# Optimization experiments

Measured on AMD Instinct MI355X. Metric: run time of the kernel, lower is better.

## Reference

```python
import jax, jax.numpy as jnp
import numpy as np

NUM_HEADS = 8
NUM_LEVELS = 4
NUM_POINTS = 16
NUM_BEV = 2
EMBED = 256
BS = 64
NQ = NUM_LEVELS * NUM_POINTS  # 64


def _bilinear_sample(img, grid):
    """F.grid_sample(mode='bilinear', padding_mode='zeros', align_corners=False).
    img: (N, C, H, W); grid: (N, Hg, Wg, 2) in [-1, 1] (x, y). Returns (N, C, Hg, Wg)."""
    N, C, H, W = img.shape
    gx = (grid[..., 0] + 1.0) * (W * 0.5) - 0.5  # (N, Hg, Wg)
    gy = (grid[..., 1] + 1.0) * (H * 0.5) - 0.5
    x0 = jnp.floor(gx)
    y0 = jnp.floor(gy)
    flat = img.reshape(N, C, H * W)

    def gather(xi, yi):
        valid = (xi >= 0) & (xi <= W - 1) & (yi >= 0) & (yi <= H - 1)
        xc = jnp.clip(xi, 0, W - 1).astype(jnp.int32)
        yc = jnp.clip(yi, 0, H - 1).astype(jnp.int32)
        idx = (yc * W + xc).reshape(N, 1, -1)
        g = jnp.take_along_axis(flat, idx, axis=2).reshape(N, C, xi.shape[1], xi.shape[2])
        return g * valid[:, None, :, :].astype(img.dtype)

    wx1 = (gx - x0)[:, None]  # (N,1,Hg,Wg)
    wy1 = (gy - y0)[:, None]
    v00 = gather(x0, y0)
    v01 = gather(x0 + 1.0, y0)
    v10 = gather(x0, y0 + 1.0)
    v11 = gather(x0 + 1.0, y0 + 1.0)
    top = v00 * (1.0 - wx1) + v01 * wx1
    bot = v10 * (1.0 - wx1) + v11 * wx1
    return top * (1.0 - wy1) + bot * wy1


def _forward(query, key_hist, value_hist, reference_points, W_off, b_off, spatial_shapes):
    bs, nq, d = query.shape
    Hn, L, P, BEV = NUM_HEADS, NUM_LEVELS, NUM_POINTS, NUM_BEV
    dh = d // Hn
    Pb = P * BEV
    ss = np.asarray(spatial_shapes)  # (L, 2) static (h, w)

    queries = jnp.concatenate([query, query], axis=1)           # (bs, 2*nq, d)
    keies = jnp.concatenate([query, key_hist], axis=1)
    values = jnp.concatenate([query, value_hist], axis=1)
    qb = queries.shape[1]

    # sampling offsets projection (the only used learned linear in the original forward)
    off = (queries @ W_off + b_off).reshape(bs, qb, Hn, Pb, L, 2)

    # NOTE: original re-assigns q/k/v from the RAW concatenated tensors (to_Q/to_K/to_V discarded)
    qh = queries.reshape(bs, qb, Hn, dh)
    kh = keies.reshape(bs, qb, Hn, dh)
    vh = values.reshape(bs, qb, Hn, dh)

    attn = jax.nn.softmax(jnp.einsum('bqhd,bkhd->bqhk', qh, kh), axis=-1)
    attn = attn.reshape(bs, qb, Hn, L, Pb)

    rp = jnp.concatenate([reference_points, reference_points], axis=1)  # (bs, qb, L, 2)
    norm = jnp.stack([jnp.asarray(ss[:, 1], jnp.float32),
                      jnp.asarray(ss[:, 0], jnp.float32)], axis=-1)      # (L, 2) = (w, h)
    loc = rp[:, :, None, None, :, :] + off / norm                        # (bs,qb,H,Pb,L,2)
    # FAITHFUL: original uses .view here (pure reshape, not a transpose)
    loc = loc.reshape(bs, qb, Hn, L, Pb, 2)
    grids = 2.0 * loc - 1.0

    sampled = []
    start = 0
    for l in range(L):
        h_, w_ = int(ss[l, 0]), int(ss[l, 1])
        vl = vh[:, start:start + h_ * w_]                                # (bs, hw, H, dh)
        start += h_ * w_
        img = vl.transpose(0, 2, 3, 1).reshape(bs * Hn, dh, h_, w_)      # (bs*H, dh, h, w)
        grid_l = grids[:, :, :, l].transpose(0, 2, 1, 3, 4).reshape(bs * Hn, qb, Pb, 2)
        sampled.append(_bilinear_sample(img, grid_l))                    # (bs*H, dh, qb, Pb)

    samp = jnp.stack(sampled, axis=-2).reshape(bs * Hn, dh, qb, L * Pb)
    aw = attn.transpose(0, 2, 1, 3, 4).reshape(bs * Hn, 1, qb, L * Pb)
    out = (samp * aw).sum(-1)                                            # (bs*H, dh, qb)
    # FAITHFUL: original reshapes q_bev dim as (nq, BEV) and means over BEV
    out = out.reshape(bs, Hn * dh, nq, BEV).mean(-1).transpose(0, 2, 1)  # (bs, nq, d)
    return out + query  # dropout is identity at eval


def setup_inputs() -> dict:
    key = jax.random.key(0)
    ks = jax.random.split(key, 6)
    query = jax.random.normal(ks[0], (BS, NQ, EMBED), jnp.float32)
    key_hist = jax.random.normal(ks[1], (BS, NQ, EMBED), jnp.float32)
    value_hist = jax.random.normal(ks[2], (BS, NQ, EMBED), jnp.float32)
    reference_points = jax.random.uniform(ks[3], (BS, NQ, NUM_LEVELS, 2), jnp.float32)
    spatial_shapes = jnp.array([[4, 8]] * NUM_LEVELS, dtype=jnp.int32)  # sum(h*w)=128=L*P*BEV
    off_dim = NUM_HEADS * NUM_BEV * NUM_POINTS * NUM_LEVELS * 2
    W_off = jax.random.normal(ks[4], (EMBED, off_dim), jnp.float32) * 0.02
    b_off = jnp.zeros((off_dim,), jnp.float32)
    return {"query": query, "key_hist": key_hist, "value_hist": value_hist,
            "reference_points": reference_points, "spatial_shapes": spatial_shapes,
            "W_off": W_off, "b_off": b_off}


def reference(query, key_hist, value_hist, reference_points, spatial_shapes, W_off, b_off):
    return _forward(query, key_hist, value_hist, reference_points, W_off, b_off, spatial_shapes)
```

## Files before the change

kernel.cpp:

```cpp
#include <hip/hip_runtime.h>


typedef short  s16x8 __attribute__((ext_vector_type(8)));
typedef short  s16x4 __attribute__((ext_vector_type(4)));
typedef float  f32x4 __attribute__((ext_vector_type(4)));

__device__ __forceinline__ unsigned short f2bf(float f) {
    union { float f; unsigned u; } v; v.f = f;
    unsigned r = v.u + 0x7FFFu + ((v.u >> 16) & 1u);
    return (unsigned short)(r >> 16);
}

__global__ __launch_bounds__(256) void conv_bf16(const float* __restrict__ in,
                                                 short* __restrict__ out) {
    const int i4 = (blockIdx.x * 256 + threadIdx.x) * 4;
    const float4 v = *(const float4*)(in + i4);
    s16x4 o;
    o.x = (short)f2bf(v.x); o.y = (short)f2bf(v.y);
    o.z = (short)f2bf(v.z); o.w = (short)f2bf(v.w);
    *(s16x4*)(out + i4) = o;
}

__global__ __launch_bounds__(256) void transp_bf16(const float* __restrict__ W,
                                                   short* __restrict__ Wt) {
    __shared__ float s[32][33];
    const int n0 = blockIdx.x * 32, k0 = blockIdx.y * 32;
    const int c = threadIdx.x & 31, r0 = threadIdx.x >> 5;
    #pragma unroll
    for (int p = 0; p < 4; ++p) {
        const int r = r0 + p * 8;
        s[r][c] = W[(size_t)(k0 + r) * 2048 + n0 + c];
    }
    __syncthreads();
    #pragma unroll
    for (int p = 0; p < 4; ++p) {
        const int r = r0 + p * 8;
        Wt[(size_t)(n0 + r) * 256 + k0 + c] = (short)f2bf(s[c][r]);
    }
}

__global__ __launch_bounds__(256) void offs_gemm_mfma(
    const short* __restrict__ Ab, const short* __restrict__ Wt,
    const float* __restrict__ bias, short* __restrict__ OFFb)
{
    __shared__ __align__(16) short Asl[128][40];
    __shared__ __align__(16) short Bsl[128][40];
    const int n0 = blockIdx.x * 128, m0 = blockIdx.y * 128;
    const int t = threadIdx.x, lane = t & 63, wave = t >> 6;
    const int wm0 = (wave >> 1) * 64, wn0 = (wave & 1) * 64;
    const int r = lane & 15, q = lane >> 4;

    f32x4 acc[4][4] = {};

    for (int kc = 0; kc < 256; kc += 32) {
        #pragma unroll
        for (int ss = 0; ss < 2; ++ss) {
            const int seg = t + ss * 256;
            const int row = seg >> 2, off8 = (seg & 3) * 8;
            *(s16x8*)&Asl[row][off8] =
                *(const s16x8*)(Ab + (size_t)(m0 + row) * 256 + kc + off8);
            *(s16x8*)&Bsl[row][off8] =
                *(const s16x8*)(Wt + (size_t)(n0 + row) * 256 + kc + off8);
        }
        __syncthreads();
        s16x8 af[4], bf[4];
        #pragma unroll
        for (int i = 0; i < 4; ++i) {
            af[i] = *(const s16x8*)&Asl[wm0 + i * 16 + r][q * 8];
            bf[i] = *(const s16x8*)&Bsl[wn0 + i * 16 + r][q * 8];
        }
        #pragma unroll
        for (int i = 0; i < 4; ++i)
            #pragma unroll
            for (int j = 0; j < 4; ++j)
                acc[i][j] = __builtin_amdgcn_mfma_f32_16x16x32_bf16(
                    af[i], bf[j], acc[i][j], 0, 0, 0);
        __syncthreads();
    }

    #pragma unroll
    for (int j = 0; j < 4; ++j) {
        const int col = n0 + wn0 + j * 16 + r;
        const float bb = bias[col];
        #pragma unroll
        for (int i = 0; i < 4; ++i) {
            const int rowg = m0 + wm0 + i * 16 + q * 4;
            #pragma unroll
            for (int rg = 0; rg < 4; ++rg)
                OFFb[(size_t)(rowg + rg) * 2048 + col] =
                    (short)f2bf(acc[i][j][rg] + bb);
        }
    }
}

__global__ __launch_bounds__(256, 2) void fused_tsa(
    const float* __restrict__ query, const float* __restrict__ key_hist,
    const float* __restrict__ value_hist, const float* __restrict__ refp,
    const unsigned short* __restrict__ OFFb, float* __restrict__ out)
{
    const int h  = blockIdx.x;
    const int b  = blockIdx.y;
    const int s  = blockIdx.z;
    const int q0 = s * 32;
    const int t  = threadIdx.x;

    __shared__ float pool[32 * 128 + 32 * 32];
    __shared__ float vs[128][36];
    __shared__ float att[32][128];
    __shared__ float rps[32][8];
    __shared__ float red[32][8];
    __shared__ float rowmax[32];
    __shared__ float invsum[32];

    float (*ks_t)[128] = (float (*)[128])pool;
    float (*qs_t)[32]  = (float (*)[32])(pool + 4096);
    float (*Am)[132]   = (float (*)[132])pool;

    {
        const int q = t & 31, v4 = t >> 5;
        const float4 v = *(const float4*)(query +
            (size_t)(b * 64 + q0 + q) * 256 + h * 32 + v4 * 4);
        qs_t[v4 * 4 + 0][q] = v.x; qs_t[v4 * 4 + 1][q] = v.y;
        qs_t[v4 * 4 + 2][q] = v.z; qs_t[v4 * 4 + 3][q] = v.w;
    }
    {
        const int kq = t & 31, v4 = t >> 5;
        #pragma unroll
        for (int p = 0; p < 4; ++p) {
            const int krow = p * 32 + kq;
            const size_t roff = (krow < 64)
                ? (size_t)(b * 64 + krow) * 256
                : (size_t)(b * 64 + krow - 64) * 256;
            const float* srck = (krow < 64) ? query : key_hist;
            const float* srcv = (krow < 64) ? query : value_hist;
            const float4 kv = *(const float4*)(srck + roff + h * 32 + v4 * 4);
            ks_t[v4 * 4 + 0][krow] = kv.x; ks_t[v4 * 4 + 1][krow] = kv.y;
            ks_t[v4 * 4 + 2][krow] = kv.z; ks_t[v4 * 4 + 3][krow] = kv.w;
            *(float4*)(&vs[krow][v4 * 4]) =
                *(const float4*)(srcv + roff + h * 32 + v4 * 4);
        }
    }
    {
        const int q = t >> 3, j = t & 7;
        rps[q][j] = refp[(size_t)(b * 64 + q0 + q) * 8 + j];
    }
    __syncthreads();

    {
        const int qt = (t >> 5) * 4;
        const int kt = (t & 31) * 4;
        float accl[4][4] = {};
        #pragma unroll
        for (int dd = 0; dd < 32; ++dd) {
            const float4 qv = *(const float4*)(&qs_t[dd][qt]);
            const float4 kv = *(const float4*)(&ks_t[dd][kt]);
            const float qa[4] = {qv.x, qv.y, qv.z, qv.w};
            const float ka[4] = {kv.x, kv.y, kv.z, kv.w};
            #pragma unroll
            for (int i = 0; i < 4; ++i)
                #pragma unroll
                for (int j = 0; j < 4; ++j)
                    accl[i][j] += qa[i] * ka[j];
        }
        #pragma unroll
        for (int i = 0; i < 4; ++i)
            #pragma unroll
            for (int j = 0; j < 4; ++j)
                att[qt + i][kt + j] = accl[i][j];
    }
    __syncthreads();

    for (int idx = t; idx < 32 * 132; idx += 256) pool[idx] = 0.f;

    {
        const int q = t >> 3, part = t & 7;
        const int k0 = part * 16;
        float m = -1e30f;
        #pragma unroll
        for (int k = 0; k < 16; ++k) m = fmaxf(m, att[q][k0 + k]);
        red[q][part] = m;
        __syncthreads();
        if (part == 0) {
            float M = red[q][0];
            #pragma unroll
            for (int p = 1; p < 8; ++p) M = fmaxf(M, red[q][p]);
            rowmax[q] = M;
        }
        __syncthreads();
        const float M = rowmax[q];
        float ssum = 0.f;
        #pragma unroll
        for (int k = 0; k < 16; ++k) {
            const float e = __expf(att[q][k0 + k] - M);
            att[q][k0 + k] = e;
            ssum += e;
        }
        red[q][part] = ssum;
        __syncthreads();
        if (part == 0) {
            float S = red[q][0];
            #pragma unroll
            for (int p = 1; p < 8; ++p) S += red[q][p];
            invsum[q] = 1.0f / S;
        }
        __syncthreads();
    }

    {
        const int q = t >> 3, fg = t & 7;
        const unsigned int* offrow = (const unsigned int*)(OFFb +
            (size_t)(b * 64 + q0 + q) * 2048 + h * 256);
        const float isum = invsum[q];
        float* row = Am[q];
        for (int i = 0; i < 16; ++i) {
            const int f = fg + 8 * i;
            const unsigned int u = offrow[f];
            const float oxv = __uint_as_float(u << 16);
            const float oyv = __uint_as_float(u & 0xFFFF0000u);
            const float a = att[q][f] * isum;
            const int l = f & 3;
            const float locx = rps[q][l * 2 + 0] + oxv * 0.125f;
            const float locy = rps[q][l * 2 + 1] + oyv * 0.25f;
            const float gx = 8.f * locx - 0.5f;
            const float gy = 4.f * locy - 0.5f;
            const float x0f = floorf(gx), y0f = floorf(gy);
            const float wx = gx - x0f, wy = gy - y0f;
            const int x0 = (int)x0f, y0 = (int)y0f;
            const int base = (f >> 5) * 32;
            const bool xv0 = (x0 >= 0) && (x0 < 8);
            const bool xv1 = (x0 >= -1) && (x0 < 7);
            const bool yv0 = (y0 >= 0) && (y0 < 4);
            const bool yv1 = (y0 >= -1) && (y0 < 3);
            if (xv0 && yv0) atomicAdd(&row[base + y0 * 8 + x0],           a * (1.f - wx) * (1.f - wy));
            if (xv1 && yv0) atomicAdd(&row[base + y0 * 8 + x0 + 1],       a * wx * (1.f - wy));
            if (xv0 && yv1) atomicAdd(&row[base + (y0 + 1) * 8 + x0],     a * (1.f - wx) * wy);
            if (xv1 && yv1) atomicAdd(&row[base + (y0 + 1) * 8 + x0 + 1], a * wx * wy);
        }
    }
    __syncthreads();

    {
        const int d4 = (t & 7) * 4;
        const int q  = t >> 3;
        float acc[4] = {0.f, 0.f, 0.f, 0.f};
        #pragma unroll 4
        for (int p = 0; p < 128; ++p) {
            const float a = Am[q][p];
            const float4 v = *(const float4*)(&vs[p][d4]);
            acc[0] += a * v.x; acc[1] += a * v.y;
            acc[2] += a * v.z; acc[3] += a * v.w;
        }
        float avg[4];
        #pragma unroll
        for (int j = 0; j < 4; ++j)
            avg[j] = 0.5f * (acc[j] + __shfl_xor(acc[j], 8, 64));
        const int qg  = q0 + q;
        const int pj  = qg >> 1;
        const int row = (qg & 1) ? (pj + 32) : pj;
        const float4 qv = *(const float4*)(query +
            (size_t)(b * 64 + row) * 256 + h * 32 + d4);
        float4 o;
        o.x = qv.x + avg[0]; o.y = qv.y + avg[1];
        o.z = qv.z + avg[2]; o.w = qv.w + avg[3];
        *(float4*)(out + (size_t)(b * 64 + row) * 256 + h * 32 + d4) = o;
    }
}

extern "C" void kernel_launch(void* const* d_in, const int* in_sizes, int n_in,
                              void* d_out, int out_size, void* d_ws, size_t ws_size,
                              hipStream_t stream) {
    (void)in_sizes; (void)n_in; (void)out_size; (void)ws_size;
    const float* query      = (const float*)d_in[0];
    const float* key_hist   = (const float*)d_in[1];
    const float* value_hist = (const float*)d_in[2];
    const float* refp       = (const float*)d_in[3];
    const float* W_off      = (const float*)d_in[5];
    const float* b_off      = (const float*)d_in[6];

    char* ws = (char*)d_ws;
    short* Ab   = (short*)(ws);
    short* Wt   = (short*)(ws + (2u << 20));
    short* OFFb = (short*)(ws + (3u << 20));
    float* out  = (float*)d_out;

    conv_bf16<<<1024, 256, 0, stream>>>(query, Ab);
    transp_bf16<<<dim3(64, 8), 256, 0, stream>>>(W_off, Wt);
    offs_gemm_mfma<<<dim3(16, 32), 256, 0, stream>>>(Ab, Wt, b_off, OFFb);
    fused_tsa<<<dim3(8, 64, 2), 256, 0, stream>>>(query, key_hist, value_hist,
                                                  refp, (const unsigned short*)OFFb,
                                                  out);
}
```

Measured before the change: 178.4 us.

## Restructure pipeline: MFMA attention and value GEMM, fused W conversion, staged stores

The two prep kernels are merged into one. It converts query and key_hist to bf16 and builds a transposed bf16 copy of the values. The offset GEMM now reads fp32 W directly, converting and transposing it in-tile, and writes its output through LDS so global stores are coalesced. The main kernel handles all 64 queries per (batch, head) block and computes QK^T and the sample-weighted value product with MFMA bf16 instructions, doing the softmax in registers with shuffles. This removes the scalar FP32 dot-product loops and several syncs, at the cost of reduced precision in scores and values and a fresh W conversion in every GEMM block.

New measurement: 187.3 us. 5.0% more time.

```diff
diff --git a/kernel.cpp b/kernel.cpp
--- a/kernel.cpp
+++ b/kernel.cpp
@@ -11,40 +11,51 @@
     return (unsigned short)(r >> 16);
 }
 
-__global__ __launch_bounds__(256) void conv_bf16(const float* __restrict__ in,
-                                                 short* __restrict__ out) {
-    const int i4 = (blockIdx.x * 256 + threadIdx.x) * 4;
-    const float4 v = *(const float4*)(in + i4);
-    s16x4 o;
-    o.x = (short)f2bf(v.x); o.y = (short)f2bf(v.y);
-    o.z = (short)f2bf(v.z); o.w = (short)f2bf(v.w);
-    *(s16x4*)(out + i4) = o;
-}
-
-__global__ __launch_bounds__(256) void transp_bf16(const float* __restrict__ W,
-                                                   short* __restrict__ Wt) {
-    __shared__ float s[32][33];
-    const int n0 = blockIdx.x * 32, k0 = blockIdx.y * 32;
-    const int c = threadIdx.x & 31, r0 = threadIdx.x >> 5;
-    #pragma unroll
-    for (int p = 0; p < 4; ++p) {
-        const int r = r0 + p * 8;
-        s[r][c] = W[(size_t)(k0 + r) * 2048 + n0 + c];
-    }
-    __syncthreads();
-    #pragma unroll
-    for (int p = 0; p < 4; ++p) {
-        const int r = r0 + p * 8;
-        Wt[(size_t)(n0 + r) * 256 + k0 + c] = (short)f2bf(s[c][r]);
+__global__ __launch_bounds__(256) void prep(
+    const float* __restrict__ query, const float* __restrict__ key_hist,
+    const float* __restrict__ value_hist,
+    short* __restrict__ Ab, short* __restrict__ Khb, short* __restrict__ VTg)
+{
+    const int job = blockIdx.x, t = threadIdx.x;
+    if (job < 2048) {
+        const bool isK = job >= 1024;
+        const float* src = isK ? key_hist : query;
+        short* dst = isK ? Khb : Ab;
+        const int i4 = ((job & 1023) * 256 + t) * 4;
+        const float4 v = *(const float4*)(src + i4);
+        s16x4 o;
+        o.x = (short)f2bf(v.x); o.y = (short)f2bf(v.y);
+        o.z = (short)f2bf(v.z); o.w = (short)f2bf(v.w);
+        *(s16x4*)(dst + i4) = o;
+    } else {
+        const int bh = job - 2048;
+        const int b = bh >> 3, h = bh & 7;
+        #pragma unroll
+        for (int pass = 0; pass < 4; ++pass) {
+            const int idx = t + 256 * pass;
+            const int p = idx >> 3;
+            const int dg = idx & 7;
+            const float* src = (p < 64) ? query : value_hist;
+            const float4 v = *(const float4*)(src +
+                (size_t)(b * 64 + (p & 63)) * 256 + h * 32 + dg * 4);
+            short* o = VTg + ((size_t)bh * 32 + dg * 4) * 128 + p;
+            o[0 * 128] = (short)f2bf(v.x);
+            o[1 * 128] = (short)f2bf(v.y);
+            o[2 * 128] = (short)f2bf(v.z);
+            o[3 * 128] = (short)f2bf(v.w);
+        }
     }
 }
 
 __global__ __launch_bounds__(256) void offs_gemm_mfma(
-    const short* __restrict__ Ab, const short* __restrict__ Wt,
+    const short* __restrict__ Ab, const float* __restrict__ W,
     const float* __restrict__ bias, short* __restrict__ OFFb)
 {
-    __shared__ __align__(16) short Asl[128][40];
-    __shared__ __align__(16) short Bsl[128][40];
+    __shared__ __align__(16) short smem[128 * 136];
+    short (*Asl)[40] = (short (*)[40])smem;
+    short (*Bsl)[40] = (short (*)[40])(smem + 128 * 40);
+    short (*Cst)[136] = (short (*)[136])smem;
+
     const int n0 = blockIdx.x * 128, m0 = blockIdx.y * 128;
     const int t = threadIdx.x, lane = t & 63, wave = t >> 6;
     const int wm0 = (wave >> 1) * 64, wn0 = (wave & 1) * 64;
@@ -59,8 +70,16 @@
             const int row = seg >> 2, off8 = (seg & 3) * 8;
             *(s16x8*)&Asl[row][off8] =
                 *(const s16x8*)(Ab + (size_t)(m0 + row) * 256 + kc + off8);
-            *(s16x8*)&Bsl[row][off8] =
-                *(const s16x8*)(Wt + (size_t)(n0 + row) * 256 + kc + off8);
+        }
+        #pragma unroll
+        for (int i = 0; i < 4; ++i) {
+            const int slot = t + 256 * i;
+            const int kk = slot >> 5, n4 = (slot & 31) * 4;
+            const float4 w4 = *(const float4*)(W + (size_t)(kc + kk) * 2048 + n0 + n4);
+            Bsl[n4 + 0][kk] = (short)f2bf(w4.x);
+            Bsl[n4 + 1][kk] = (short)f2bf(w4.y);
+            Bsl[n4 + 2][kk] = (short)f2bf(w4.z);
+            Bsl[n4 + 3][kk] = (short)f2bf(w4.w);
         }
         __syncthreads();
         s16x8 af[4], bf[4];
@@ -80,189 +99,171 @@
 
     #pragma unroll
     for (int j = 0; j < 4; ++j) {
-        const int col = n0 + wn0 + j * 16 + r;
-        const float bb = bias[col];
-        #pragma unroll
-        for (int i = 0; i < 4; ++i) {
-            const int rowg = m0 + wm0 + i * 16 + q * 4;
+        const float bb = bias[n0 + wn0 + j * 16 + r];
+        #pragma unroll
+        for (int i = 0; i < 4; ++i)
             #pragma unroll
             for (int rg = 0; rg < 4; ++rg)
-                OFFb[(size_t)(rowg + rg) * 2048 + col] =
+                Cst[wm0 + i * 16 + q * 4 + rg][wn0 + j * 16 + r] =
                     (short)f2bf(acc[i][j][rg] + bb);
-        }
-    }
-}
-
-__global__ __launch_bounds__(256, 2) void fused_tsa(
-    const float* __restrict__ query, const float* __restrict__ key_hist,
-    const float* __restrict__ value_hist, const float* __restrict__ refp,
-    const unsigned short* __restrict__ OFFb, float* __restrict__ out)
+    }
+    __syncthreads();
+    {
+        const int row = t >> 1, half = t & 1;
+        short* gdst = OFFb + (size_t)(m0 + row) * 2048 + n0 + half * 64;
+        const short* lsrc = &Cst[row][half * 64];
+        #pragma unroll
+        for (int u = 0; u < 8; ++u)
+            *(s16x8*)(gdst + u * 8) = *(const s16x8*)(lsrc + u * 8);
+    }
+}
+
+__global__ __launch_bounds__(256) void fused_tsa2(
+    const float* __restrict__ query, const float* __restrict__ refp,
+    const short* __restrict__ Ab, const short* __restrict__ Khb,
+    const short* __restrict__ VTg, const unsigned* __restrict__ OFFu,
+    float* __restrict__ out)
 {
-    const int h  = blockIdx.x;
-    const int b  = blockIdx.y;
-    const int s  = blockIdx.z;
-    const int q0 = s * 32;
-    const int t  = threadIdx.x;
-
-    __shared__ float pool[32 * 128 + 32 * 32];
-    __shared__ float vs[128][36];
-    __shared__ float att[32][128];
-    __shared__ float rps[32][8];
-    __shared__ float red[32][8];
-    __shared__ float rowmax[32];
-    __shared__ float invsum[32];
-
-    float (*ks_t)[128] = (float (*)[128])pool;
-    float (*qs_t)[32]  = (float (*)[32])(pool + 4096);
-    float (*Am)[132]   = (float (*)[132])pool;
-
-    {
-        const int q = t & 31, v4 = t >> 5;
-        const float4 v = *(const float4*)(query +
-            (size_t)(b * 64 + q0 + q) * 256 + h * 32 + v4 * 4);
-        qs_t[v4 * 4 + 0][q] = v.x; qs_t[v4 * 4 + 1][q] = v.y;
-        qs_t[v4 * 4 + 2][q] = v.z; qs_t[v4 * 4 + 3][q] = v.w;
-    }
-    {
-        const int kq = t & 31, v4 = t >> 5;
-        #pragma unroll
-        for (int p = 0; p < 4; ++p) {
-            const int krow = p * 32 + kq;
-            const size_t roff = (krow < 64)
-                ? (size_t)(b * 64 + krow) * 256
-                : (size_t)(b * 64 + krow - 64) * 256;
-            const float* srck = (krow < 64) ? query : key_hist;
-            const float* srcv = (krow < 64) ? query : value_hist;
-            const float4 kv = *(const float4*)(srck + roff + h * 32 + v4 * 4);
-            ks_t[v4 * 4 + 0][krow] = kv.x; ks_t[v4 * 4 + 1][krow] = kv.y;
-            ks_t[v4 * 4 + 2][krow] = kv.z; ks_t[v4 * 4 + 3][krow] = kv.w;
-            *(float4*)(&vs[krow][v4 * 4]) =
-                *(const float4*)(srcv + roff + h * 32 + v4 * 4);
-        }
-    }
-    {
-        const int q = t >> 3, j = t & 7;
-        rps[q][j] = refp[(size_t)(b * 64 + q0 + q) * 8 + j];
-    }
-    __syncthreads();
-
-    {
-        const int qt = (t >> 5) * 4;
-        const int kt = (t & 31) * 4;
-        float accl[4][4] = {};
-        #pragma unroll
-        for (int dd = 0; dd < 32; ++dd) {
-            const float4 qv = *(const float4*)(&qs_t[dd][qt]);
-            const float4 kv = *(const float4*)(&ks_t[dd][kt]);
-            const float qa[4] = {qv.x, qv.y, qv.z, qv.w};
-            const float ka[4] = {kv.x, kv.y, kv.z, kv.w};
-            #pragma unroll
-            for (int i = 0; i < 4; ++i)
-                #pragma unroll
-                for (int j = 0; j < 4; ++j)
-                    accl[i][j] += qa[i] * ka[j];
-        }
-        #pragma unroll
-        for (int i = 0; i < 4; ++i)
-            #pragma unroll
-            for (int j = 0; j < 4; ++j)
-                att[qt + i][kt + j] = accl[i][j];
-    }
-    __syncthreads();
-
-    for (int idx = t; idx < 32 * 132; idx += 256) pool[idx] = 0.f;
-
-    {
-        const int q = t >> 3, part = t & 7;
-        const int k0 = part * 16;
-        float m = -1e30f;
-        #pragma unroll
-        for (int k = 0; k < 16; ++k) m = fmaxf(m, att[q][k0 + k]);
-        red[q][part] = m;
-        __syncthreads();
-        if (part == 0) {
-            float M = red[q][0];
-            #pragma unroll
-            for (int p = 1; p < 8; ++p) M = fmaxf(M, red[q][p]);
-            rowmax[q] = M;
-        }
-        __syncthreads();
-        const float M = rowmax[q];
+    const int h = blockIdx.x, b = blockIdx.y;
+    const int t = threadIdx.x, lane = t & 63, wave = t >> 6;
+    const int quad = lane >> 4, col = lane & 15;
+    const int wq = wave * 16;
+
+    __shared__ __align__(16) float Am[64][132];
+    short* Amb = (short*)&Am[0][0];
+
+    unsigned off_u[8][4];
+    {
+        const unsigned* ob = OFFu + ((size_t)b * 64 + wq + quad * 4) * 1024 + h * 128 + col;
+        #pragma unroll
+        for (int r = 0; r < 4; ++r)
+            #pragma unroll
+            for (int t8 = 0; t8 < 8; ++t8)
+                off_u[t8][r] = ob[r * 1024 + t8 * 16];
+    }
+    float rpx[4], rpy[4];
+    #pragma unroll
+    for (int r = 0; r < 4; ++r) {
+        const float2 rp = *(const float2*)(refp +
+            ((size_t)b * 64 + wq + quad * 4 + r) * 8 + (lane & 3) * 2);
+        rpx[r] = rp.x; rpy[r] = rp.y;
+    }
+
+    {
+        const int zq = t >> 2, zc = (t & 3) * 32;
+        const float4 z = {0.f, 0.f, 0.f, 0.f};
+        #pragma unroll
+        for (int u = 0; u < 8; ++u) *(float4*)&Am[zq][zc + 4 * u] = z;
+    }
+
+    const s16x8 aq = *(const s16x8*)(Ab +
+        ((size_t)b * 64 + wq + col) * 256 + h * 32 + quad * 8);
+    f32x4 acc[8];
+    #pragma unroll
+    for (int t8 = 0; t8 < 8; ++t8) {
+        const int n = t8 * 16 + col;
+        const short* src = (t8 < 4)
+            ? (Ab  + ((size_t)b * 64 + n) * 256)
+            : (Khb + ((size_t)b * 64 + n - 64) * 256);
+        const s16x8 bk = *(const s16x8*)(src + h * 32 + quad * 8);
+        const f32x4 z = {0.f, 0.f, 0.f, 0.f};
+        acc[t8] = __builtin_amdgcn_mfma_f32_16x16x32_bf16(aq, bk, z, 0, 0, 0);
+    }
+
+    float att[8][4];
+    #pragma unroll
+    for (int r = 0; r < 4; ++r) {
+        float m = acc[0][r];
+        #pragma unroll
+        for (int t8 = 1; t8 < 8; ++t8) m = fmaxf(m, acc[t8][r]);
+        #pragma unroll
+        for (int s = 1; s < 16; s <<= 1) m = fmaxf(m, __shfl_xor(m, s, 64));
         float ssum = 0.f;
         #pragma unroll
-        for (int k = 0; k < 16; ++k) {
-            const float e = __expf(att[q][k0 + k] - M);
-            att[q][k0 + k] = e;
-            ssum += e;
-        }
-        red[q][part] = ssum;
-        __syncthreads();
-        if (part == 0) {
-            float S = red[q][0];
-            #pragma unroll
-            for (int p = 1; p < 8; ++p) S += red[q][p];
-            invsum[q] = 1.0f / S;
-        }
-        __syncthreads();
-    }
-
-    {
-        const int q = t >> 3, fg = t & 7;
-        const unsigned int* offrow = (const unsigned int*)(OFFb +
-            (size_t)(b * 64 + q0 + q) * 2048 + h * 256);
-        const float isum = invsum[q];
-        float* row = Am[q];
-        for (int i = 0; i < 16; ++i) {
-            const int f = fg + 8 * i;
-            const unsigned int u = offrow[f];
-            const float oxv = __uint_as_float(u << 16);
-            const float oyv = __uint_as_float(u & 0xFFFF0000u);
-            const float a = att[q][f] * isum;
-            const int l = f & 3;
-            const float locx = rps[q][l * 2 + 0] + oxv * 0.125f;
-            const float locy = rps[q][l * 2 + 1] + oyv * 0.25f;
-            const float gx = 8.f * locx - 0.5f;
-            const float gy = 4.f * locy - 0.5f;
+        for (int t8 = 0; t8 < 8; ++t8) {
+            const float e = __expf(acc[t8][r] - m);
+            att[t8][r] = e; ssum += e;
+        }
+        #pragma unroll
+        for (int s = 1; s < 16; s <<= 1) ssum += __shfl_xor(ssum, s, 64);
+        const float inv = 1.0f / ssum;
+        #pragma unroll
+        for (int t8 = 0; t8 < 8; ++t8) att[t8][r] *= inv;
+    }
+    __syncthreads();
+
+    #pragma unroll
+    for (int t8 = 0; t8 < 8; ++t8) {
+        const int f = col + 16 * t8;
+        const int base = (f >> 5) * 32;
+        #pragma unroll
+        for (int r = 0; r < 4; ++r) {
+            float* rowW = &Am[wq + quad * 4 + r][0];
+            const float a = att[t8][r];
+            const unsigned u = off_u[t8][r];
+            const float ox = __uint_as_float(u << 16);
+            const float oy = __uint_as_float(u & 0xFFFF0000u);
+            const float gx = 8.f * (rpx[r] + ox * 0.125f) - 0.5f;
+            const float gy = 4.f * (rpy[r] + oy * 0.25f) - 0.5f;
             const float x0f = floorf(gx), y0f = floorf(gy);
             const float wx = gx - x0f, wy = gy - y0f;
             const int x0 = (int)x0f, y0 = (int)y0f;
-            const int base = (f >> 5) * 32;
             const bool xv0 = (x0 >= 0) && (x0 < 8);
             const bool xv1 = (x0 >= -1) && (x0 < 7);
             const bool yv0 = (y0 >= 0) && (y0 < 4);
             const bool yv1 = (y0 >= -1) && (y0 < 3);
-            if (xv0 && yv0) atomicAdd(&row[base + y0 * 8 + x0],           a * (1.f - wx) * (1.f - wy));
-            if (xv1 && yv0) atomicAdd(&row[base + y0 * 8 + x0 + 1],       a * wx * (1.f - wy));
-            if (xv0 && yv1) atomicAdd(&row[base + (y0 + 1) * 8 + x0],     a * (1.f - wx) * wy);
-            if (xv1 && yv1) atomicAdd(&row[base + (y0 + 1) * 8 + x0 + 1], a * wx * wy);
-        }
-    }
-    __syncthreads();
-
-    {
-        const int d4 = (t & 7) * 4;
-        const int q  = t >> 3;
-        float acc[4] = {0.f, 0.f, 0.f, 0.f};
-        #pragma unroll 4
-        for (int p = 0; p < 128; ++p) {
-            const float a = Am[q][p];
-            const float4 v = *(const float4*)(&vs[p][d4]);
-            acc[0] += a * v.x; acc[1] += a * v.y;
-            acc[2] += a * v.z; acc[3] += a * v.w;
-        }
-        float avg[4];
-        #pragma unroll
-        for (int j = 0; j < 4; ++j)
-            avg[j] = 0.5f * (acc[j] + __shfl_xor(acc[j], 8, 64));
-        const int qg  = q0 + q;
-        const int pj  = qg >> 1;
-        const int row = (qg & 1) ? (pj + 32) : pj;
-        const float4 qv = *(const float4*)(query +
-            (size_t)(b * 64 + row) * 256 + h * 32 + d4);
-        float4 o;
-        o.x = qv.x + avg[0]; o.y = qv.y + avg[1];
-        o.z = qv.z + avg[2]; o.w = qv.w + avg[3];
-        *(float4*)(out + (size_t)(b * 64 + row) * 256 + h * 32 + d4) = o;
+            if (xv0 && yv0) atomicAdd(&rowW[base + y0 * 8 + x0],           a * (1.f - wx) * (1.f - wy));
+            if (xv1 && yv0) atomicAdd(&rowW[base + y0 * 8 + x0 + 1],       a * wx * (1.f - wy));
+            if (xv0 && yv1) atomicAdd(&rowW[base + (y0 + 1) * 8 + x0],     a * (1.f - wx) * wy);
+            if (xv1 && yv1) atomicAdd(&rowW[base + (y0 + 1) * 8 + x0 + 1], a * wx * wy);
+        }
+    }
+    __syncthreads();
+
+    {
+        const int cq = t >> 2, cc = (t & 3) * 32;
+        float vreg[32];
+        #pragma unroll
+        for (int u = 0; u < 8; ++u) {
+            const float4 v = *(const float4*)&Am[cq][cc + 4 * u];
+            vreg[4 * u + 0] = v.x; vreg[4 * u + 1] = v.y;
+            vreg[4 * u + 2] = v.z; vreg[4 * u + 3] = v.w;
+        }
+        __syncthreads();
+        #pragma unroll
+        for (int u = 0; u < 4; ++u) {
+            s16x8 o;
+            #pragma unroll
+            for (int j = 0; j < 8; ++j) o[j] = (short)f2bf(vreg[u * 8 + j]);
+            *(s16x8*)&Amb[cq * 136 + cc + u * 8] = o;
+        }
+    }
+    __syncthreads();
+
+    f32x4 oacc[2] = {};
+    #pragma unroll
+    for (int ks = 0; ks < 4; ++ks) {
+        const s16x8 af = *(const s16x8*)&Amb[(wq + col) * 136 + ks * 32 + quad * 8];
+        #pragma unroll
+        for (int n2 = 0; n2 < 2; ++n2) {
+            const s16x8 bv = *(const s16x8*)(VTg +
+                ((size_t)(b * 8 + h) * 32 + n2 * 16 + col) * 128 + ks * 32 + quad * 8);
+            oacc[n2] = __builtin_amdgcn_mfma_f32_16x16x32_bf16(af, bv, oacc[n2], 0, 0, 0);
+        }
+    }
+
+    #pragma unroll
+    for (int n2 = 0; n2 < 2; ++n2) {
+        const int d = h * 32 + n2 * 16 + col;
+        #pragma unroll
+        for (int pr = 0; pr < 2; ++pr) {
+            const float avg = 0.5f * (oacc[n2][2 * pr] + oacc[n2][2 * pr + 1]);
+            const int pj = wave * 8 + quad * 2 + pr;
+            const size_t re = ((size_t)b * 64 + pj) * 256 + d;
+            const size_t ro = ((size_t)b * 64 + pj + 32) * 256 + d;
+            out[re] = query[re] + avg;
+            out[ro] = query[ro] + avg;
+        }
     }
 }
 
@@ -279,14 +280,13 @@
 
     char* ws = (char*)d_ws;
     short* Ab   = (short*)(ws);
-    short* Wt   = (short*)(ws + (2u << 20));
-    short* OFFb = (short*)(ws + (3u << 20));
+    short* Khb  = (short*)(ws + (2u << 20));
+    short* VTg  = (short*)(ws + (4u << 20));
+    short* OFFb = (short*)(ws + (8u << 20));
     float* out  = (float*)d_out;
 
-    conv_bf16<<<1024, 256, 0, stream>>>(query, Ab);
-    transp_bf16<<<dim3(64, 8), 256, 0, stream>>>(W_off, Wt);
-    offs_gemm_mfma<<<dim3(16, 32), 256, 0, stream>>>(Ab, Wt, b_off, OFFb);
-    fused_tsa<<<dim3(8, 64, 2), 256, 0, stream>>>(query, key_hist, value_hist,
-                                                  refp, (const unsigned short*)OFFb,
-                                                  out);
-}
+    prep<<<2560, 256, 0, stream>>>(query, key_hist, value_hist, Ab, Khb, VTg);
+    offs_gemm_mfma<<<dim3(16, 32), 256, 0, stream>>>(Ab, W_off, b_off, OFFb);
+    fused_tsa2<<<dim3(8, 64), 256, 0, stream>>>(query, refp, Ab, Khb, VTg,
+                                                (const unsigned*)OFFb, out);
+}
```
